# Kernel optimization log

Measured on AMD Instinct MI355X. Metric: run time of the kernel, lower is better.

## Reference

```python
import jax, jax.numpy as jnp
import numpy as np

L, D, DFF, B = 8192, 768, 3072, 2  # seq len, model dim, ffn hidden (4*D), batch

def _ln(x, g, b):
    m = x.mean(-1, keepdims=True)
    v = ((x - m) ** 2).mean(-1, keepdims=True)
    return (x - m) / jnp.sqrt(v + 1e-5) * g + b

def _ffn(x, w1, b1, w2, b2):
    return jax.nn.silu(x @ w1 + b1) @ w2 + b2

def setup_inputs() -> dict:
    key = jax.random.key(0)
    ks = jax.random.split(key, 8)
    s = lambda k, shape: jax.random.normal(k, shape, dtype=jnp.float32) * 0.02
    return dict(
        z=jax.random.normal(ks[0], (B, L, D), dtype=jnp.float32),
        pos=s(ks[1], (L, D)),                      # learned positional encoding table
        a=jax.random.normal(ks[2], (1,), dtype=jnp.float32),
        w1p=s(ks[3], (D, DFF)), b1p=jnp.zeros((DFF,), jnp.float32),
        w2p=s(ks[4], (DFF, D)), b2p=jnp.zeros((D,), jnp.float32),
        w1=s(ks[5], (D, DFF)),  b1=jnp.zeros((DFF,), jnp.float32),
        w2=s(ks[6], (DFF, D)),  b2=jnp.zeros((D,), jnp.float32),
        gamma=jnp.ones((D,), jnp.float32),
        beta=jnp.zeros((D,), jnp.float32),
    )

def reference(z, pos, a, w1p, b1p, w2p, b2p, w1, b1, w2, b2, gamma, beta):
    Ls = z.shape[1]
    n = 2 * Ls  # zero-padded FFT length for linear (causal) convolution
    fz = jnp.fft.rfft(_ln(z, gamma, beta), n=n, axis=1)          # (B, L+1, D) complex
    h = _ffn(pos, w1p, b1p, w2p, b2p)                            # (L, D) implicit filter
    window = jnp.exp(-jnp.arange(Ls, dtype=jnp.float32) * jnp.exp(a[0]))  # (L,)
    wfh = jnp.fft.rfft(window[:, None] * h, n=n, axis=0)         # (L+1, D) complex
    conv = jnp.fft.irfft(wfh[None] * fz, n=n, axis=1)[:, :Ls]    # (B, L, D)
    z = conv + z
    z = _ffn(_ln(z, gamma, beta), w1, b1, w2, b2) + z
    return z
```

## Files before the change

kernel.cpp:

```cpp
#include <hip/hip_runtime.h>
#include <hip/hip_bf16.h>
#include <stdint.h>

typedef __hip_bfloat16 bf16;
typedef __bf16 bf16x8 __attribute__((ext_vector_type(8)));
typedef float f32x4 __attribute__((ext_vector_type(4)));

#define LQ   8192
#define DQ   768
#define DFFQ 3072
#define NF   8192
#define NFULL 16384
#define TWO_PI 6.2831853071795864769f

__device__ __forceinline__ float b2f(bf16 v) { return __bfloat162float(v); }
__device__ __forceinline__ bf16 f2b(float v) { return __float2bfloat16(v); }
__device__ __forceinline__ float ldf(const bf16& v) { return __bfloat162float(v); }
__device__ __forceinline__ float ldf(const float& v) { return v; }
__device__ __forceinline__ float2 cmul(float2 a, float2 b) {
    return make_float2(a.x * b.x - a.y * b.y, a.x * b.y + a.y * b.x);
}
__device__ __forceinline__ int rev13(int k) { return (int)(__brev((unsigned)k) >> 19); }

__device__ __forceinline__ void glds16(const bf16* g, unsigned short* l) {
    __builtin_amdgcn_global_load_lds(
        (const __attribute__((address_space(1))) void*)g,
        (__attribute__((address_space(3))) void*)l, 16, 0, 0);
}

__global__ __launch_bounds__(256) void cast_f32_bf16(const float* __restrict__ in,
                                                     bf16* __restrict__ out, int n) {
    int i = (blockIdx.x * 256 + threadIdx.x) * 4;
    if (i + 3 < n) {
        float4 v = *(const float4*)(in + i);
        out[i] = f2b(v.x); out[i + 1] = f2b(v.y);
        out[i + 2] = f2b(v.z); out[i + 3] = f2b(v.w);
    }
}

template <typename TIN>
__global__ __launch_bounds__(256) void ln_kernel(const TIN* __restrict__ x,
                                                 const float* __restrict__ gamma,
                                                 const float* __restrict__ beta,
                                                 bf16* __restrict__ y) {
    size_t row = blockIdx.x;
    const TIN* xr = x + row * DQ;
    int tid = threadIdx.x;
    float v0 = ldf(xr[tid]), v1 = ldf(xr[tid + 256]), v2 = ldf(xr[tid + 512]);
    float s = v0 + v1 + v2;
    float sq = v0 * v0 + v1 * v1 + v2 * v2;
    for (int o = 32; o > 0; o >>= 1) {
        s += __shfl_down(s, o, 64);
        sq += __shfl_down(sq, o, 64);
    }
    __shared__ float red[8];
    __shared__ float mi[2];
    int lane = tid & 63, wid = tid >> 6;
    if (lane == 0) { red[wid] = s; red[4 + wid] = sq; }
    __syncthreads();
    if (tid == 0) {
        float ts = red[0] + red[1] + red[2] + red[3];
        float tq = red[4] + red[5] + red[6] + red[7];
        float mean = ts * (1.0f / 768.0f);
        float var = tq * (1.0f / 768.0f) - mean * mean;
        mi[0] = mean;
        mi[1] = rsqrtf(var + 1e-5f);
    }
    __syncthreads();
    float mean = mi[0], inv = mi[1];
    bf16* yr = y + row * DQ;
    yr[tid]       = f2b((v0 - mean) * inv * gamma[tid]       + beta[tid]);
    yr[tid + 256] = f2b((v1 - mean) * inv * gamma[tid + 256] + beta[tid + 256]);
    yr[tid + 512] = f2b((v2 - mean) * inv * gamma[tid + 512] + beta[tid + 512]);
}

template <typename TIN>
__global__ __launch_bounds__(256) void transpose_to_bf16(const TIN* __restrict__ in,
                                                         bf16* __restrict__ out,
                                                         int R, int C) {
    __shared__ bf16 tile[32][33];
    size_t base = (size_t)blockIdx.z * (size_t)R * (size_t)C;
    int c0 = blockIdx.x * 32, r0 = blockIdx.y * 32;
    int x = threadIdx.x, ty = threadIdx.y;
    for (int i = ty; i < 32; i += 8)
        tile[i][x] = f2b(ldf(in[base + (size_t)(r0 + i) * C + c0 + x]));
    __syncthreads();
    for (int i = ty; i < 32; i += 8)
        out[base + (size_t)(c0 + i) * R + r0 + x] = tile[x][i];
}

__global__ __launch_bounds__(256) void transpose_window(const float* __restrict__ h,
                                                        const float* __restrict__ a,
                                                        float* __restrict__ whT) {
    __shared__ float tile[32][33];
    float rate = expf(a[0]);
    int d0 = blockIdx.x * 32, t0 = blockIdx.y * 32;
    int x = threadIdx.x, ty = threadIdx.y;
    for (int i = ty; i < 32; i += 8) {
        int t = t0 + i;
        tile[i][x] = h[(size_t)t * DQ + d0 + x] * expf(-(float)t * rate);
    }
    __syncthreads();
    for (int i = ty; i < 32; i += 8)
        whT[(size_t)(d0 + i) * LQ + t0 + x] = tile[x][i];
}

__global__ __launch_bounds__(256) void transpose_residual(const bf16* __restrict__ convT,
                                                          const float* __restrict__ z,
                                                          bf16* __restrict__ z2) {
    __shared__ bf16 tile[32][33];
    size_t cbase = (size_t)blockIdx.z * DQ * LQ;
    size_t zbase = (size_t)blockIdx.z * LQ * DQ;
    int t0 = blockIdx.x * 32, d0 = blockIdx.y * 32;
    int x = threadIdx.x, ty = threadIdx.y;
    for (int i = ty; i < 32; i += 8)
        tile[i][x] = convT[cbase + (size_t)(d0 + i) * LQ + t0 + x];
    __syncthreads();
    for (int i = ty; i < 32; i += 8) {
        size_t idx = zbase + (size_t)(t0 + i) * DQ + d0 + x;
        z2[idx] = f2b(b2f(tile[x][i]) + z[idx]);
    }
}

__device__ __forceinline__ void fft_dif8192(float2* s) {
    const int tid = threadIdx.x;
    for (int half = 4096; half >= 1; half >>= 1) {
        float base = -TWO_PI / (float)(half * 2);
        for (int m = tid; m < 4096; m += 1024) {
            int j = m & (half - 1);
            int i0 = ((m - j) << 1) + j;
            int i1 = i0 + half;
            float2 u = s[i0], v = s[i1];
            float sn, cs;
            __sincosf(base * (float)j, &sn, &cs);
            s[i0] = make_float2(u.x + v.x, u.y + v.y);
            float dx = u.x - v.x, dy = u.y - v.y;
            s[i1] = make_float2(dx * cs - dy * sn, dx * sn + dy * cs);
        }
        __syncthreads();
    }
}
__device__ __forceinline__ void fft_dit8192(float2* s) {
    const int tid = threadIdx.x;
    for (int half = 1; half <= 4096; half <<= 1) {
        float base = TWO_PI / (float)(half * 2);
        for (int m = tid; m < 4096; m += 1024) {
            int j = m & (half - 1);
            int i0 = ((m - j) << 1) + j;
            int i1 = i0 + half;
            float2 u = s[i0], v = s[i1];
            float sn, cs;
            __sincosf(base * (float)j, &sn, &cs);
            float2 tv = make_float2(v.x * cs - v.y * sn, v.x * sn + v.y * cs);
            s[i0] = make_float2(u.x + tv.x, u.y + tv.y);
            s[i1] = make_float2(u.x - tv.x, u.y - tv.y);
        }
        __syncthreads();
    }
}

__global__ __launch_bounds__(1024) void filter_fft(const float* __restrict__ whT,
                                                   float2* __restrict__ H) {
    __shared__ float2 s[NF];
    int p = blockIdx.x;
    int d0 = 2 * p, d1 = d0 + 1;
    const float* x0 = whT + (size_t)d0 * LQ;
    const float* x1 = whT + (size_t)d1 * LQ;
    float2* H0 = H + (size_t)d0 * 8193;
    float2* H1 = H + (size_t)d1 * 8193;
    int tid = threadIdx.x;
    for (int t = tid; t < NF; t += 1024) s[t] = make_float2(x0[t], x1[t]);
    __syncthreads();
    fft_dif8192(s);
    for (int m = tid; m <= 4096; m += 1024) {
        int p1 = rev13(m), p2 = rev13((NF - m) & (NF - 1));
        float2 u = s[p1], v = s[p2];
        H0[2 * m] = make_float2(0.5f * (u.x + v.x), 0.5f * (u.y - v.y));
        H1[2 * m] = make_float2(0.5f * (u.y + v.y), 0.5f * (v.x - u.x));
    }
    __syncthreads();
    for (int t = tid; t < NF; t += 1024) {
        float sn, cs;
        __sincosf(-TWO_PI * (float)t / (float)NFULL, &sn, &cs);
        float2 xc = make_float2(x0[t], x1[t]);
        s[t] = make_float2(xc.x * cs - xc.y * sn, xc.x * sn + xc.y * cs);
    }
    __syncthreads();
    fft_dif8192(s);
    for (int m = tid; m < 4096; m += 1024) {
        int p1 = rev13(m), p2 = rev13(NF - 1 - m);
        float2 u = s[p1], v = s[p2];
        H0[2 * m + 1] = make_float2(0.5f * (u.x + v.x), 0.5f * (u.y - v.y));
        H1[2 * m + 1] = make_float2(0.5f * (u.y + v.y), 0.5f * (v.x - u.x));
    }
}

__global__ __launch_bounds__(1024) void fft_conv(const bf16* __restrict__ xlnT,
                                                 const float2* __restrict__ H,
                                                 bf16* __restrict__ convT) {
    __shared__ float2 s[NF];
    int wg = blockIdx.x;
    int b = wg / 384, p = wg % 384;
    int d0 = 2 * p, d1 = d0 + 1;
    const bf16* x0 = xlnT + ((size_t)b * DQ + d0) * LQ;
    const bf16* x1 = x0 + LQ;
    const float2* H0 = H + (size_t)d0 * 8193;
    const float2* H1 = H + (size_t)d1 * 8193;
    bf16* o0 = convT + ((size_t)b * DQ + d0) * LQ;
    bf16* o1 = o0 + LQ;
    int tid = threadIdx.x;

    for (int t = tid; t < NF; t += 1024) s[t] = make_float2(b2f(x0[t]), b2f(x1[t]));
    __syncthreads();
    fft_dif8192(s);
    for (int m = tid; m <= 4096; m += 1024) {
        int p1 = rev13(m), p2 = rev13((NF - m) & (NF - 1));
        float2 u = s[p1], v = s[p2];
        float2 X0 = make_float2(0.5f * (u.x + v.x), 0.5f * (u.y - v.y));
        float2 X1 = make_float2(0.5f * (u.y + v.y), 0.5f * (v.x - u.x));
        float2 Y0 = cmul(H0[2 * m], X0);
        float2 Y1 = cmul(H1[2 * m], X1);
        s[p1] = make_float2(Y0.x - Y1.y, Y0.y + Y1.x);
        s[p2] = make_float2(Y0.x + Y1.y, Y1.x - Y0.y);
    }
    __syncthreads();
    fft_dit8192(s);
    float2 e[8];
    for (int i = 0; i < 8; i++) e[i] = s[tid + 1024 * i];
    __syncthreads();

    for (int t = tid; t < NF; t += 1024) {
        float sn, cs;
        __sincosf(-TWO_PI * (float)t / (float)NFULL, &sn, &cs);
        float xv0 = b2f(x0[t]), xv1 = b2f(x1[t]);
        s[t] = make_float2(xv0 * cs - xv1 * sn, xv0 * sn + xv1 * cs);
    }
    __syncthreads();
    fft_dif8192(s);
    for (int m = tid; m < 4096; m += 1024) {
        int p1 = rev13(m), p2 = rev13(NF - 1 - m);
        float2 u = s[p1], v = s[p2];
        float2 X0 = make_float2(0.5f * (u.x + v.x), 0.5f * (u.y - v.y));
        float2 X1 = make_float2(0.5f * (u.y + v.y), 0.5f * (v.x - u.x));
        float2 Y0 = cmul(H0[2 * m + 1], X0);
        float2 Y1 = cmul(H1[2 * m + 1], X1);
        s[p1] = make_float2(Y0.x - Y1.y, Y0.y + Y1.x);
        s[p2] = make_float2(Y0.x + Y1.y, Y1.x - Y0.y);
    }
    __syncthreads();
    fft_dit8192(s);
    const float sc = 1.0f / (float)NFULL;
    for (int i = 0; i < 8; i++) {
        int t = tid + 1024 * i;
        float sn, cs;
        __sincosf(TWO_PI * (float)t / (float)NFULL, &sn, &cs);
        float2 o = s[t];
        float2 ot = make_float2(o.x * cs - o.y * sn, o.x * sn + o.y * cs);
        o0[t] = f2b((e[i].x + ot.x) * sc);
        o1[t] = f2b((e[i].y + ot.y) * sc);
    }
}

#define BMT 128
#define BNT 128
#define BKT 32

template <int EPI>
__global__ __launch_bounds__(256) void gemm_bt(const bf16* __restrict__ A,
                                               const bf16* __restrict__ Bt,
                                               const float* __restrict__ bias,
                                               const bf16* __restrict__ res,
                                               void* __restrict__ out,
                                               int M, int N, int K) {
    __shared__ __align__(16) unsigned short As[BMT * BKT];
    __shared__ __align__(16) unsigned short Bs[BNT * BKT];
    int tid = threadIdx.x;
    int m0 = blockIdx.y * BMT, n0 = blockIdx.x * BNT;
    int lane = tid & 63, w = tid >> 6;
    int wm = w >> 1, wn = w & 1;
    int colq = lane & 15, quad = lane >> 4;

    f32x4 acc[4][4];
    for (int i = 0; i < 4; i++)
        for (int j = 0; j < 4; j++) acc[i][j] = (f32x4){0.f, 0.f, 0.f, 0.f};

    int lrow = lane >> 2, lcol = (lane & 3) * 8;
    int ch0 = w * 2, ch1 = w * 2 + 1;
    const bf16* ga0 = A + (size_t)(m0 + ch0 * 16 + lrow) * K + lcol;
    const bf16* ga1 = A + (size_t)(m0 + ch1 * 16 + lrow) * K + lcol;
    const bf16* gb0 = Bt + (size_t)(n0 + ch0 * 16 + lrow) * K + lcol;
    const bf16* gb1 = Bt + (size_t)(n0 + ch1 * 16 + lrow) * K + lcol;
    unsigned short* la0 = As + ch0 * 512;
    unsigned short* la1 = As + ch1 * 512;
    unsigned short* lb0 = Bs + ch0 * 512;
    unsigned short* lb1 = Bs + ch1 * 512;

    const int nk = K / BKT;
    for (int kb = 0; kb < nk; kb++) {
        int k0 = kb * BKT;
        __syncthreads();
        glds16(ga0 + k0, la0);
        glds16(ga1 + k0, la1);
        glds16(gb0 + k0, lb0);
        glds16(gb1 + k0, lb1);
        __syncthreads();
        bf16x8 af[4], bfr[4];
        for (int i = 0; i < 4; i++) {
            int mrow = wm * 64 + i * 16 + colq;
            af[i] = *(const bf16x8*)(&As[mrow * BKT + quad * 8]);
            int nrow = wn * 64 + i * 16 + colq;
            bfr[i] = *(const bf16x8*)(&Bs[nrow * BKT + quad * 8]);
        }
        for (int i = 0; i < 4; i++)
            for (int j = 0; j < 4; j++)
                acc[i][j] = __builtin_amdgcn_mfma_f32_16x16x32_bf16(af[i], bfr[j], acc[i][j], 0, 0, 0);
    }
    for (int j = 0; j < 4; j++) {
        int n = n0 + wn * 64 + j * 16 + colq;
        float bv = bias[n];
        for (int i = 0; i < 4; i++) {
            int mbase = m0 + wm * 64 + i * 16 + quad * 4;
            for (int r = 0; r < 4; r++) {
                int m = mbase + r;
                float v = acc[i][j][r] + bv;
                size_t idx = (size_t)m * N + n;
                if (EPI == 0) {
                    ((bf16*)out)[idx] = f2b(v / (1.0f + expf(-v)));
                } else if (EPI == 1) {
                    ((float*)out)[idx] = v;
                } else {
                    ((float*)out)[idx] = v + b2f(res[idx]);
                }
            }
        }
    }
}

extern "C" void kernel_launch(void* const* d_in, const int* in_sizes, int n_in,
                              void* d_out, int out_size, void* d_ws, size_t ws_size,
                              hipStream_t stream) {
    (void)in_sizes; (void)n_in; (void)out_size; (void)ws_size;
    const float* z     = (const float*)d_in[0];
    const float* pos   = (const float*)d_in[1];
    const float* a     = (const float*)d_in[2];
    const float* w1p   = (const float*)d_in[3];
    const float* b1p   = (const float*)d_in[4];
    const float* w2p   = (const float*)d_in[5];
    const float* b2p   = (const float*)d_in[6];
    const float* w1    = (const float*)d_in[7];
    const float* b1    = (const float*)d_in[8];
    const float* w2    = (const float*)d_in[9];
    const float* b2    = (const float*)d_in[10];
    const float* gamma = (const float*)d_in[11];
    const float* beta  = (const float*)d_in[12];
    float* out = (float*)d_out;
    char* ws = (char*)d_ws;

    bf16*   w1T   = (bf16*)  (ws + 0);
    bf16*   w2T   = (bf16*)  (ws + 4718592);
    bf16*   w1pT  = (bf16*)  (ws + 9437184);
    bf16*   w2pT  = (bf16*)  (ws + 14155776);
    bf16*   xlnT  = (bf16*)  (ws + 18874368);
    bf16*   act1  = (bf16*)  (ws + 44040192);
    float2* Hbuf  = (float2*)(ws + 44040192);
    bf16*   xln   = (bf16*)  (ws + 94377984);
    bf16*   posb  = (bf16*)  (ws + 119543808);
    float*  h     = (float*) (ws + 119543808);
    float*  whT   = (float*) (ws + 94377984);
    bf16*   convT = (bf16*)  (ws + 119543808);
    bf16*   z2    = (bf16*)  (ws + 94377984);
    bf16*   xb    = (bf16*)  (ws + 119543808);
    bf16*   act2  = (bf16*)  (ws + 18874368);

    dim3 tb(32, 8);
    transpose_to_bf16<float><<<dim3(DFFQ / 32, DQ / 32, 1), tb, 0, stream>>>(w1p, w1pT, DQ, DFFQ);
    transpose_to_bf16<float><<<dim3(DQ / 32, DFFQ / 32, 1), tb, 0, stream>>>(w2p, w2pT, DFFQ, DQ);
    transpose_to_bf16<float><<<dim3(DFFQ / 32, DQ / 32, 1), tb, 0, stream>>>(w1, w1T, DQ, DFFQ);
    transpose_to_bf16<float><<<dim3(DQ / 32, DFFQ / 32, 1), tb, 0, stream>>>(w2, w2T, DFFQ, DQ);
    cast_f32_bf16<<<(LQ * DQ / 4 + 255) / 256, 256, 0, stream>>>(pos, posb, LQ * DQ);
    ln_kernel<float><<<2 * LQ, 256, 0, stream>>>(z, gamma, beta, xln);
    transpose_to_bf16<bf16><<<dim3(DQ / 32, LQ / 32, 2), tb, 0, stream>>>(xln, xlnT, LQ, DQ);
    gemm_bt<0><<<dim3(DFFQ / BNT, LQ / BMT), 256, 0, stream>>>(posb, w1pT, b1p, nullptr, act1, LQ, DFFQ, DQ);
    gemm_bt<1><<<dim3(DQ / BNT, LQ / BMT), 256, 0, stream>>>(act1, w2pT, b2p, nullptr, h, LQ, DQ, DFFQ);
    transpose_window<<<dim3(DQ / 32, LQ / 32), tb, 0, stream>>>(h, a, whT);
    filter_fft<<<DQ / 2, 1024, 0, stream>>>(whT, Hbuf);
    fft_conv<<<2 * (DQ / 2), 1024, 0, stream>>>(xlnT, Hbuf, convT);
    transpose_residual<<<dim3(LQ / 32, DQ / 32, 2), tb, 0, stream>>>(convT, z, z2);
    ln_kernel<bf16><<<2 * LQ, 256, 0, stream>>>(z2, gamma, beta, xb);
    for (int b = 0; b < 2; b++) {
        const bf16* xbh = xb + (size_t)b * LQ * DQ;
        const bf16* z2h = z2 + (size_t)b * LQ * DQ;
        float* outh = out + (size_t)b * LQ * DQ;
        gemm_bt<0><<<dim3(DFFQ / BNT, LQ / BMT), 256, 0, stream>>>(xbh, w1T, b1, nullptr, act2, LQ, DFFQ, DQ);
        gemm_bt<2><<<dim3(DQ / BNT, LQ / BMT), 256, 0, stream>>>(act2, w2T, b2, z2h, outh, LQ, DQ, DFFQ);
    }
}
```

Measured before the change: 937.5 us.

## Replace radix-2 FFT stages with register radix-8 passes and swizzled LDS

Replaces the 13-stage radix-2 shared-memory FFT (one barrier and one LDS round trip per stage) with four radix-8 register passes plus a final shuffle-based radix-2 stage. Inputs and outputs stay in registers across the first and last passes. LDS indices are XOR-swizzled to avoid bank conflicts, and per-element sincos calls are replaced by a twiddle recurrence. The H spectrum is stored split into even and odd halves instead of interleaved. Barrier and LDS traffic drop sharply, in exchange for more register pressure and more complex indexing in a 1024-thread block.

```diff
diff --git a/kernel.cpp b/kernel.cpp
--- a/kernel.cpp
+++ b/kernel.cpp
@@ -12,6 +12,9 @@
 #define NF   8192
 #define NFULL 16384
 #define TWO_PI 6.2831853071795864769f
+#define RSQ2 0.70710678118654752f
+#define C16  0.92387953251128676f
+#define S16  0.38268343236508977f
 
 __device__ __forceinline__ float b2f(bf16 v) { return __bfloat162float(v); }
 __device__ __forceinline__ bf16 f2b(float v) { return __float2bfloat16(v); }
@@ -20,7 +23,11 @@
 __device__ __forceinline__ float2 cmul(float2 a, float2 b) {
     return make_float2(a.x * b.x - a.y * b.y, a.x * b.y + a.y * b.x);
 }
+__device__ __forceinline__ float2 csqr(float2 a) {
+    return make_float2(a.x * a.x - a.y * a.y, 2.f * a.x * a.y);
+}
 __device__ __forceinline__ int rev13(int k) { return (int)(__brev((unsigned)k) >> 19); }
+__device__ __forceinline__ int SWZ(int i) { return i ^ ((i >> 5) & 31) ^ ((i >> 9) & 15); }
 
 __device__ __forceinline__ void glds16(const bf16* g, unsigned short* l) {
     __builtin_amdgcn_global_load_lds(
@@ -122,40 +129,147 @@
     }
 }
 
-__device__ __forceinline__ void fft_dif8192(float2* s) {
+
+__device__ __forceinline__ void dif_bf(float2& u, float2& v, float2 tw) {
+    float2 a = make_float2(u.x + v.x, u.y + v.y);
+    float2 b = make_float2(u.x - v.x, u.y - v.y);
+    u = a; v = cmul(b, tw);
+}
+__device__ __forceinline__ void dit_bf(float2& u, float2& v, float2 tw) {
+    float2 tv = cmul(v, tw);
+    v = make_float2(u.x - tv.x, u.y - tv.y);
+    u = make_float2(u.x + tv.x, u.y + tv.y);
+}
+
+__device__ __forceinline__ void dif3(float2* x, float2 w) {
+    float2 w2 = csqr(w), w4 = csqr(w2);
+    float2 t1 = cmul(w, make_float2(RSQ2, -RSQ2));
+    float2 t2 = make_float2(w.y, -w.x);
+    float2 t3 = cmul(w, make_float2(-RSQ2, -RSQ2));
+    dif_bf(x[0], x[4], w);
+    dif_bf(x[1], x[5], t1);
+    dif_bf(x[2], x[6], t2);
+    dif_bf(x[3], x[7], t3);
+    float2 w2n = make_float2(w2.y, -w2.x);
+    dif_bf(x[0], x[2], w2);
+    dif_bf(x[1], x[3], w2n);
+    dif_bf(x[4], x[6], w2);
+    dif_bf(x[5], x[7], w2n);
+    dif_bf(x[0], x[1], w4);
+    dif_bf(x[2], x[3], w4);
+    dif_bf(x[4], x[5], w4);
+    dif_bf(x[6], x[7], w4);
+}
+__device__ __forceinline__ void dit3(float2* x, float2 w) {
+    float2 w2 = csqr(w), w4 = csqr(w2);
+    dit_bf(x[0], x[1], w4);
+    dit_bf(x[2], x[3], w4);
+    dit_bf(x[4], x[5], w4);
+    dit_bf(x[6], x[7], w4);
+    float2 w2p = make_float2(-w2.y, w2.x);
+    dit_bf(x[0], x[2], w2);
+    dit_bf(x[1], x[3], w2p);
+    dit_bf(x[4], x[6], w2);
+    dit_bf(x[5], x[7], w2p);
+    float2 t1 = cmul(w, make_float2(RSQ2, RSQ2));
+    float2 t2 = make_float2(-w.y, w.x);
+    float2 t3 = cmul(w, make_float2(-RSQ2, RSQ2));
+    dit_bf(x[0], x[4], w);
+    dit_bf(x[1], x[5], t1);
+    dit_bf(x[2], x[6], t2);
+    dit_bf(x[3], x[7], t3);
+}
+
+__device__ __forceinline__ void shfl_stage(float2* x, int l) {
+#pragma unroll
+    for (int i = 0; i < 8; i++) {
+        float ox = __shfl_xor(x[i].x, 1, 64);
+        float oy = __shfl_xor(x[i].y, 1, 64);
+        if (l == 0) { x[i].x += ox; x[i].y += oy; }
+        else        { x[i].x = ox - x[i].x; x[i].y = oy - x[i].y; }
+    }
+}
+
+__device__ __forceinline__ void fwd_fft(float2* s, float2* x) {
     const int tid = threadIdx.x;
-    for (int half = 4096; half >= 1; half >>= 1) {
-        float base = -TWO_PI / (float)(half * 2);
-        for (int m = tid; m < 4096; m += 1024) {
-            int j = m & (half - 1);
-            int i0 = ((m - j) << 1) + j;
-            int i1 = i0 + half;
-            float2 u = s[i0], v = s[i1];
-            float sn, cs;
-            __sincosf(base * (float)j, &sn, &cs);
-            s[i0] = make_float2(u.x + v.x, u.y + v.y);
-            float dx = u.x - v.x, dy = u.y - v.y;
-            s[i1] = make_float2(dx * cs - dy * sn, dx * sn + dy * cs);
-        }
-        __syncthreads();
-    }
-}
-__device__ __forceinline__ void fft_dit8192(float2* s) {
+    float sn, cs;
+    __sincosf(-(TWO_PI / 8192.f) * (float)tid, &sn, &cs);
+    dif3(x, make_float2(cs, sn));
+#pragma unroll
+    for (int i = 0; i < 8; i++) s[SWZ(tid + 1024 * i)] = x[i];
+    __syncthreads();
+    {
+        int l = tid & 127, base = (tid >> 7) * 1024 + l;
+#pragma unroll
+        for (int i = 0; i < 8; i++) x[i] = s[SWZ(base + 128 * i)];
+        __sincosf(-(TWO_PI / 1024.f) * (float)l, &sn, &cs);
+        dif3(x, make_float2(cs, sn));
+#pragma unroll
+        for (int i = 0; i < 8; i++) s[SWZ(base + 128 * i)] = x[i];
+    }
+    __syncthreads();
+    {
+        int l = tid & 15, base = (tid >> 4) * 128 + l;
+#pragma unroll
+        for (int i = 0; i < 8; i++) x[i] = s[SWZ(base + 16 * i)];
+        __sincosf(-(TWO_PI / 128.f) * (float)l, &sn, &cs);
+        dif3(x, make_float2(cs, sn));
+#pragma unroll
+        for (int i = 0; i < 8; i++) s[SWZ(base + 16 * i)] = x[i];
+    }
+    __syncthreads();
+    {
+        int l = tid & 1, base = (tid >> 1) * 16 + l;
+#pragma unroll
+        for (int i = 0; i < 8; i++) x[i] = s[SWZ(base + 2 * i)];
+        float2 w = l ? make_float2(C16, -S16) : make_float2(1.f, 0.f);
+        dif3(x, w);
+        shfl_stage(x, l);
+#pragma unroll
+        for (int i = 0; i < 8; i++) s[SWZ(base + 2 * i)] = x[i];
+    }
+    __syncthreads();
+}
+
+__device__ __forceinline__ void inv_fft(float2* s, float2* x) {
     const int tid = threadIdx.x;
-    for (int half = 1; half <= 4096; half <<= 1) {
-        float base = TWO_PI / (float)(half * 2);
-        for (int m = tid; m < 4096; m += 1024) {
-            int j = m & (half - 1);
-            int i0 = ((m - j) << 1) + j;
-            int i1 = i0 + half;
-            float2 u = s[i0], v = s[i1];
-            float sn, cs;
-            __sincosf(base * (float)j, &sn, &cs);
-            float2 tv = make_float2(v.x * cs - v.y * sn, v.x * sn + v.y * cs);
-            s[i0] = make_float2(u.x + tv.x, u.y + tv.y);
-            s[i1] = make_float2(u.x - tv.x, u.y - tv.y);
-        }
-        __syncthreads();
+    float sn, cs;
+    {
+        int l = tid & 1, base = (tid >> 1) * 16 + l;
+#pragma unroll
+        for (int i = 0; i < 8; i++) x[i] = s[SWZ(base + 2 * i)];
+        shfl_stage(x, l);
+        float2 w = l ? make_float2(C16, S16) : make_float2(1.f, 0.f);
+        dit3(x, w);
+#pragma unroll
+        for (int i = 0; i < 8; i++) s[SWZ(base + 2 * i)] = x[i];
+    }
+    __syncthreads();
+    {
+        int l = tid & 15, base = (tid >> 4) * 128 + l;
+#pragma unroll
+        for (int i = 0; i < 8; i++) x[i] = s[SWZ(base + 16 * i)];
+        __sincosf((TWO_PI / 128.f) * (float)l, &sn, &cs);
+        dit3(x, make_float2(cs, sn));
+#pragma unroll
+        for (int i = 0; i < 8; i++) s[SWZ(base + 16 * i)] = x[i];
+    }
+    __syncthreads();
+    {
+        int l = tid & 127, base = (tid >> 7) * 1024 + l;
+#pragma unroll
+        for (int i = 0; i < 8; i++) x[i] = s[SWZ(base + 128 * i)];
+        __sincosf((TWO_PI / 1024.f) * (float)l, &sn, &cs);
+        dit3(x, make_float2(cs, sn));
+#pragma unroll
+        for (int i = 0; i < 8; i++) s[SWZ(base + 128 * i)] = x[i];
+    }
+    __syncthreads();
+    {
+#pragma unroll
+        for (int i = 0; i < 8; i++) x[i] = s[SWZ(tid + 1024 * i)];
+        __sincosf((TWO_PI / 8192.f) * (float)tid, &sn, &cs);
+        dit3(x, make_float2(cs, sn));
     }
 }
 
@@ -169,29 +283,38 @@
     float2* H0 = H + (size_t)d0 * 8193;
     float2* H1 = H + (size_t)d1 * 8193;
     int tid = threadIdx.x;
-    for (int t = tid; t < NF; t += 1024) s[t] = make_float2(x0[t], x1[t]);
-    __syncthreads();
-    fft_dif8192(s);
+    float2 x[8];
+#pragma unroll
+    for (int i = 0; i < 8; i++) {
+        int t = tid + 1024 * i;
+        x[i] = make_float2(x0[t], x1[t]);
+    }
+    fwd_fft(s, x);
     for (int m = tid; m <= 4096; m += 1024) {
-        int p1 = rev13(m), p2 = rev13((NF - m) & (NF - 1));
+        int p1 = SWZ(rev13(m)), p2 = SWZ(rev13((NF - m) & (NF - 1)));
         float2 u = s[p1], v = s[p2];
-        H0[2 * m] = make_float2(0.5f * (u.x + v.x), 0.5f * (u.y - v.y));
-        H1[2 * m] = make_float2(0.5f * (u.y + v.y), 0.5f * (v.x - u.x));
-    }
-    __syncthreads();
-    for (int t = tid; t < NF; t += 1024) {
+        H0[m] = make_float2(0.5f * (u.x + v.x), 0.5f * (u.y - v.y));
+        H1[m] = make_float2(0.5f * (u.y + v.y), 0.5f * (v.x - u.x));
+    }
+    __syncthreads();
+    {
         float sn, cs;
-        __sincosf(-TWO_PI * (float)t / (float)NFULL, &sn, &cs);
-        float2 xc = make_float2(x0[t], x1[t]);
-        s[t] = make_float2(xc.x * cs - xc.y * sn, xc.x * sn + xc.y * cs);
-    }
-    __syncthreads();
-    fft_dif8192(s);
+        __sincosf(-(TWO_PI / 16384.f) * (float)tid, &sn, &cs);
+        float2 ch = make_float2(cs, sn);
+        const float2 stepm = make_float2(C16, -S16);
+#pragma unroll
+        for (int i = 0; i < 8; i++) {
+            int t = tid + 1024 * i;
+            x[i] = cmul(make_float2(x0[t], x1[t]), ch);
+            ch = cmul(ch, stepm);
+        }
+    }
+    fwd_fft(s, x);
     for (int m = tid; m < 4096; m += 1024) {
-        int p1 = rev13(m), p2 = rev13(NF - 1 - m);
+        int p1 = SWZ(rev13(m)), p2 = SWZ(rev13(NF - 1 - m));
         float2 u = s[p1], v = s[p2];
-        H0[2 * m + 1] = make_float2(0.5f * (u.x + v.x), 0.5f * (u.y - v.y));
-        H1[2 * m + 1] = make_float2(0.5f * (u.y + v.y), 0.5f * (v.x - u.x));
+        H0[4097 + m] = make_float2(0.5f * (u.x + v.x), 0.5f * (u.y - v.y));
+        H1[4097 + m] = make_float2(0.5f * (u.y + v.y), 0.5f * (v.x - u.x));
     }
 }
 
@@ -209,55 +332,70 @@
     bf16* o0 = convT + ((size_t)b * DQ + d0) * LQ;
     bf16* o1 = o0 + LQ;
     int tid = threadIdx.x;
-
-    for (int t = tid; t < NF; t += 1024) s[t] = make_float2(b2f(x0[t]), b2f(x1[t]));
-    __syncthreads();
-    fft_dif8192(s);
+    float2 x[8];
+
+#pragma unroll
+    for (int i = 0; i < 8; i++) {
+        int t = tid + 1024 * i;
+        x[i] = make_float2(b2f(x0[t]), b2f(x1[t]));
+    }
+    fwd_fft(s, x);
     for (int m = tid; m <= 4096; m += 1024) {
-        int p1 = rev13(m), p2 = rev13((NF - m) & (NF - 1));
+        int p1 = SWZ(rev13(m)), p2 = SWZ(rev13((NF - m) & (NF - 1)));
         float2 u = s[p1], v = s[p2];
         float2 X0 = make_float2(0.5f * (u.x + v.x), 0.5f * (u.y - v.y));
         float2 X1 = make_float2(0.5f * (u.y + v.y), 0.5f * (v.x - u.x));
-        float2 Y0 = cmul(H0[2 * m], X0);
-        float2 Y1 = cmul(H1[2 * m], X1);
+        float2 Y0 = cmul(H0[m], X0);
+        float2 Y1 = cmul(H1[m], X1);
         s[p1] = make_float2(Y0.x - Y1.y, Y0.y + Y1.x);
         s[p2] = make_float2(Y0.x + Y1.y, Y1.x - Y0.y);
     }
     __syncthreads();
-    fft_dit8192(s);
+    inv_fft(s, x);
     float2 e[8];
-    for (int i = 0; i < 8; i++) e[i] = s[tid + 1024 * i];
-    __syncthreads();
-
-    for (int t = tid; t < NF; t += 1024) {
+#pragma unroll
+    for (int i = 0; i < 8; i++) e[i] = x[i];
+    __syncthreads();
+
+    {
         float sn, cs;
-        __sincosf(-TWO_PI * (float)t / (float)NFULL, &sn, &cs);
-        float xv0 = b2f(x0[t]), xv1 = b2f(x1[t]);
-        s[t] = make_float2(xv0 * cs - xv1 * sn, xv0 * sn + xv1 * cs);
-    }
-    __syncthreads();
-    fft_dif8192(s);
+        __sincosf(-(TWO_PI / 16384.f) * (float)tid, &sn, &cs);
+        float2 ch = make_float2(cs, sn);
+        const float2 stepm = make_float2(C16, -S16);
+#pragma unroll
+        for (int i = 0; i < 8; i++) {
+            int t = tid + 1024 * i;
+            x[i] = cmul(make_float2(b2f(x0[t]), b2f(x1[t])), ch);
+            ch = cmul(ch, stepm);
+        }
+    }
+    fwd_fft(s, x);
     for (int m = tid; m < 4096; m += 1024) {
-        int p1 = rev13(m), p2 = rev13(NF - 1 - m);
+        int p1 = SWZ(rev13(m)), p2 = SWZ(rev13(NF - 1 - m));
         float2 u = s[p1], v = s[p2];
         float2 X0 = make_float2(0.5f * (u.x + v.x), 0.5f * (u.y - v.y));
         float2 X1 = make_float2(0.5f * (u.y + v.y), 0.5f * (v.x - u.x));
-        float2 Y0 = cmul(H0[2 * m + 1], X0);
-        float2 Y1 = cmul(H1[2 * m + 1], X1);
+        float2 Y0 = cmul(H0[4097 + m], X0);
+        float2 Y1 = cmul(H1[4097 + m], X1);
         s[p1] = make_float2(Y0.x - Y1.y, Y0.y + Y1.x);
         s[p2] = make_float2(Y0.x + Y1.y, Y1.x - Y0.y);
     }
     __syncthreads();
-    fft_dit8192(s);
-    const float sc = 1.0f / (float)NFULL;
-    for (int i = 0; i < 8; i++) {
-        int t = tid + 1024 * i;
+    inv_fft(s, x);
+    {
         float sn, cs;
-        __sincosf(TWO_PI * (float)t / (float)NFULL, &sn, &cs);
-        float2 o = s[t];
-        float2 ot = make_float2(o.x * cs - o.y * sn, o.x * sn + o.y * cs);
-        o0[t] = f2b((e[i].x + ot.x) * sc);
-        o1[t] = f2b((e[i].y + ot.y) * sc);
+        __sincosf((TWO_PI / 16384.f) * (float)tid, &sn, &cs);
+        float2 wr = make_float2(cs, sn);
+        const float2 stepp = make_float2(C16, S16);
+        const float sc = 1.0f / (float)NFULL;
+#pragma unroll
+        for (int i = 0; i < 8; i++) {
+            int t = tid + 1024 * i;
+            float2 ot = cmul(x[i], wr);
+            o0[t] = f2b((e[i].x + ot.x) * sc);
+            o1[t] = f2b((e[i].y + ot.y) * sc);
+            wr = cmul(wr, stepp);
+        }
     }
 }
 
```

Result: slower. 1.028 ms (+9.6%).

## Replace split 8192-point FFTs with single radix-4 16384-point FFT in shared memory

Applied to the files above, without the earlier changes.

Replaces the two half-length 8192-point FFT passes (even and odd bins) with one 16384-point FFT held in 128 KB of LDS. The transform uses radix-4 (two fused radix-2) stages and exploits the zero padding in the first forward and last inverse stage. An XOR swizzle on LDS indices is meant to cut bank conflicts. This roughly halves the number of barrier-separated stages and twiddle computations per convolution, but doubles LDS use per block, which may limit occupancy to one block per CU.

```diff
diff --git a/kernel.cpp b/kernel.cpp
--- a/kernel.cpp
+++ b/kernel.cpp
@@ -9,7 +9,6 @@
 #define LQ   8192
 #define DQ   768
 #define DFFQ 3072
-#define NF   8192
 #define NFULL 16384
 #define TWO_PI 6.2831853071795864769f
 
@@ -20,7 +19,11 @@
 __device__ __forceinline__ float2 cmul(float2 a, float2 b) {
     return make_float2(a.x * b.x - a.y * b.y, a.x * b.y + a.y * b.x);
 }
-__device__ __forceinline__ int rev13(int k) { return (int)(__brev((unsigned)k) >> 19); }
+__device__ __forceinline__ float2 csqr(float2 a) {
+    return make_float2(a.x * a.x - a.y * a.y, 2.f * a.x * a.y);
+}
+__device__ __forceinline__ int rev14(int k) { return (int)(__brev((unsigned)k) >> 18); }
+__device__ __forceinline__ int SWZ(int i) { return i ^ ((i >> 5) & 31) ^ ((i >> 9) & 15); }
 
 __device__ __forceinline__ void glds16(const bf16* g, unsigned short* l) {
     __builtin_amdgcn_global_load_lds(
@@ -122,38 +125,80 @@
     }
 }
 
-__device__ __forceinline__ void fft_dif8192(float2* s) {
+
+__device__ __forceinline__ void dif_bf(float2& u, float2& v, float2 tw) {
+    float2 a = make_float2(u.x + v.x, u.y + v.y);
+    float2 b = make_float2(u.x - v.x, u.y - v.y);
+    u = a; v = cmul(b, tw);
+}
+__device__ __forceinline__ void dit_bf(float2& u, float2& v, float2 tw) {
+    float2 tv = cmul(v, tw);
+    v = make_float2(u.x - tv.x, u.y - tv.y);
+    u = make_float2(u.x + tv.x, u.y + tv.y);
+}
+__device__ __forceinline__ void dif2(float2& x0, float2& x1, float2& x2, float2& x3,
+                                     float2 w) {
+    float2 w2 = csqr(w);
+    float2 wn = make_float2(w.y, -w.x);
+    dif_bf(x0, x2, w);
+    dif_bf(x1, x3, wn);
+    dif_bf(x0, x1, w2);
+    dif_bf(x2, x3, w2);
+}
+__device__ __forceinline__ void dit2(float2& x0, float2& x1, float2& x2, float2& x3,
+                                     float2 w) {
+    float2 w2 = csqr(w);
+    float2 wp = make_float2(-w.y, w.x);
+    dit_bf(x0, x1, w2);
+    dit_bf(x2, x3, w2);
+    dit_bf(x0, x2, w);
+    dit_bf(x1, x3, wp);
+}
+
+__device__ __forceinline__ void fwd_mid(float2* s) {
     const int tid = threadIdx.x;
-    for (int half = 4096; half >= 1; half >>= 1) {
-        float base = -TWO_PI / (float)(half * 2);
-        for (int m = tid; m < 4096; m += 1024) {
-            int j = m & (half - 1);
-            int i0 = ((m - j) << 1) + j;
-            int i1 = i0 + half;
-            float2 u = s[i0], v = s[i1];
-            float sn, cs;
-            __sincosf(base * (float)j, &sn, &cs);
-            s[i0] = make_float2(u.x + v.x, u.y + v.y);
-            float dx = u.x - v.x, dy = u.y - v.y;
-            s[i1] = make_float2(dx * cs - dy * sn, dx * sn + dy * cs);
+#pragma unroll
+    for (int k = 10; k >= 0; k -= 2) {
+        const int S = 1 << k;
+        for (int g2 = 0; g2 < 4; g2++) {
+            int G = tid + (g2 << 10);
+            int l = G & (S - 1);
+            int base = ((G >> k) << (k + 2)) | l;
+            float2 x0 = s[SWZ(base)];
+            float2 x1 = s[SWZ(base + S)];
+            float2 x2 = s[SWZ(base + 2 * S)];
+            float2 x3 = s[SWZ(base + 3 * S)];
+            float ang = -(TWO_PI * 0.25f / (float)S) * (float)l;
+            float2 w = make_float2(__cosf(ang), __sinf(ang));
+            dif2(x0, x1, x2, x3, w);
+            s[SWZ(base)] = x0;
+            s[SWZ(base + S)] = x1;
+            s[SWZ(base + 2 * S)] = x2;
+            s[SWZ(base + 3 * S)] = x3;
         }
         __syncthreads();
     }
 }
-__device__ __forceinline__ void fft_dit8192(float2* s) {
+__device__ __forceinline__ void inv_mid(float2* s) {
     const int tid = threadIdx.x;
-    for (int half = 1; half <= 4096; half <<= 1) {
-        float base = TWO_PI / (float)(half * 2);
-        for (int m = tid; m < 4096; m += 1024) {
-            int j = m & (half - 1);
-            int i0 = ((m - j) << 1) + j;
-            int i1 = i0 + half;
-            float2 u = s[i0], v = s[i1];
-            float sn, cs;
-            __sincosf(base * (float)j, &sn, &cs);
-            float2 tv = make_float2(v.x * cs - v.y * sn, v.x * sn + v.y * cs);
-            s[i0] = make_float2(u.x + tv.x, u.y + tv.y);
-            s[i1] = make_float2(u.x - tv.x, u.y - tv.y);
+#pragma unroll
+    for (int k = 0; k <= 10; k += 2) {
+        const int S = 1 << k;
+        for (int g2 = 0; g2 < 4; g2++) {
+            int G = tid + (g2 << 10);
+            int l = G & (S - 1);
+            int base = ((G >> k) << (k + 2)) | l;
+            float2 x0 = s[SWZ(base)];
+            float2 x1 = s[SWZ(base + S)];
+            float2 x2 = s[SWZ(base + 2 * S)];
+            float2 x3 = s[SWZ(base + 3 * S)];
+            float ang = (TWO_PI * 0.25f / (float)S) * (float)l;
+            float2 w = make_float2(__cosf(ang), __sinf(ang));
+            dit2(x0, x1, x2, x3, w);
+            s[SWZ(base)] = x0;
+            s[SWZ(base + S)] = x1;
+            s[SWZ(base + 2 * S)] = x2;
+            s[SWZ(base + 3 * S)] = x3;
         }
         __syncthreads();
     }
@@ -161,103 +206,111 @@
 
 __global__ __launch_bounds__(1024) void filter_fft(const float* __restrict__ whT,
                                                    float2* __restrict__ H) {
-    __shared__ float2 s[NF];
+    __shared__ float2 s[NFULL];
     int p = blockIdx.x;
     int d0 = 2 * p, d1 = d0 + 1;
-    const float* x0 = whT + (size_t)d0 * LQ;
-    const float* x1 = whT + (size_t)d1 * LQ;
+    const float* g0 = whT + (size_t)d0 * LQ;
+    const float* g1 = whT + (size_t)d1 * LQ;
     float2* H0 = H + (size_t)d0 * 8193;
     float2* H1 = H + (size_t)d1 * 8193;
-    int tid = threadIdx.x;
-    for (int t = tid; t < NF; t += 1024) s[t] = make_float2(x0[t], x1[t]);
-    __syncthreads();
-    fft_dif8192(s);
-    for (int m = tid; m <= 4096; m += 1024) {
-        int p1 = rev13(m), p2 = rev13((NF - m) & (NF - 1));
+    const int tid = threadIdx.x;
+
+    for (int g2 = 0; g2 < 4; g2++) {
+        int G = tid + (g2 << 10);
+        float2 x0 = make_float2(g0[G], g1[G]);
+        float2 x1 = make_float2(g0[G + 4096], g1[G + 4096]);
+        float ang = -(TWO_PI / 16384.f) * (float)G;
+        float2 w = make_float2(__cosf(ang), __sinf(ang));
+        float2 w2 = csqr(w);
+        float2 wn = make_float2(w.y, -w.x);
+        float2 x2 = cmul(x0, w);
+        float2 x3 = cmul(x1, wn);
+        dif_bf(x0, x1, w2);
+        dif_bf(x2, x3, w2);
+        s[SWZ(G)] = x0;
+        s[SWZ(G + 4096)] = x1;
+        s[SWZ(G + 8192)] = x2;
+        s[SWZ(G + 12288)] = x3;
+    }
+    __syncthreads();
+    fwd_mid(s);
+    for (int m = tid; m <= 8192; m += 1024) {
+        int p1 = SWZ(rev14(m)), p2 = SWZ(rev14((NFULL - m) & (NFULL - 1)));
         float2 u = s[p1], v = s[p2];
-        H0[2 * m] = make_float2(0.5f * (u.x + v.x), 0.5f * (u.y - v.y));
-        H1[2 * m] = make_float2(0.5f * (u.y + v.y), 0.5f * (v.x - u.x));
-    }
-    __syncthreads();
-    for (int t = tid; t < NF; t += 1024) {
-        float sn, cs;
-        __sincosf(-TWO_PI * (float)t / (float)NFULL, &sn, &cs);
-        float2 xc = make_float2(x0[t], x1[t]);
-        s[t] = make_float2(xc.x * cs - xc.y * sn, xc.x * sn + xc.y * cs);
-    }
-    __syncthreads();
-    fft_dif8192(s);
-    for (int m = tid; m < 4096; m += 1024) {
-        int p1 = rev13(m), p2 = rev13(NF - 1 - m);
-        float2 u = s[p1], v = s[p2];
-        H0[2 * m + 1] = make_float2(0.5f * (u.x + v.x), 0.5f * (u.y - v.y));
-        H1[2 * m + 1] = make_float2(0.5f * (u.y + v.y), 0.5f * (v.x - u.x));
+        H0[m] = make_float2(0.5f * (u.x + v.x), 0.5f * (u.y - v.y));
+        H1[m] = make_float2(0.5f * (u.y + v.y), 0.5f * (v.x - u.x));
     }
 }
 
 __global__ __launch_bounds__(1024) void fft_conv(const bf16* __restrict__ xlnT,
                                                  const float2* __restrict__ H,
                                                  bf16* __restrict__ convT) {
-    __shared__ float2 s[NF];
+    __shared__ float2 s[NFULL];
     int wg = blockIdx.x;
     int b = wg / 384, p = wg % 384;
     int d0 = 2 * p, d1 = d0 + 1;
-    const bf16* x0 = xlnT + ((size_t)b * DQ + d0) * LQ;
-    const bf16* x1 = x0 + LQ;
+    const bf16* g0 = xlnT + ((size_t)b * DQ + d0) * LQ;
+    const bf16* g1 = g0 + LQ;
     const float2* H0 = H + (size_t)d0 * 8193;
     const float2* H1 = H + (size_t)d1 * 8193;
     bf16* o0 = convT + ((size_t)b * DQ + d0) * LQ;
     bf16* o1 = o0 + LQ;
-    int tid = threadIdx.x;
-
-    for (int t = tid; t < NF; t += 1024) s[t] = make_float2(b2f(x0[t]), b2f(x1[t]));
-    __syncthreads();
-    fft_dif8192(s);
-    for (int m = tid; m <= 4096; m += 1024) {
-        int p1 = rev13(m), p2 = rev13((NF - m) & (NF - 1));
+    const int tid = threadIdx.x;
+
+    for (int g2 = 0; g2 < 4; g2++) {
+        int G = tid + (g2 << 10);
+        float2 x0 = make_float2(b2f(g0[G]), b2f(g1[G]));
+        float2 x1 = make_float2(b2f(g0[G + 4096]), b2f(g1[G + 4096]));
+        float ang = -(TWO_PI / 16384.f) * (float)G;
+        float2 w = make_float2(__cosf(ang), __sinf(ang));
+        float2 w2 = csqr(w);
+        float2 wn = make_float2(w.y, -w.x);
+        float2 x2 = cmul(x0, w);
+        float2 x3 = cmul(x1, wn);
+        dif_bf(x0, x1, w2);
+        dif_bf(x2, x3, w2);
+        s[SWZ(G)] = x0;
+        s[SWZ(G + 4096)] = x1;
+        s[SWZ(G + 8192)] = x2;
+        s[SWZ(G + 12288)] = x3;
+    }
+    __syncthreads();
+    fwd_mid(s);
+
+    for (int m = tid; m <= 8192; m += 1024) {
+        int p1 = SWZ(rev14(m)), p2 = SWZ(rev14((NFULL - m) & (NFULL - 1)));
         float2 u = s[p1], v = s[p2];
         float2 X0 = make_float2(0.5f * (u.x + v.x), 0.5f * (u.y - v.y));
         float2 X1 = make_float2(0.5f * (u.y + v.y), 0.5f * (v.x - u.x));
-        float2 Y0 = cmul(H0[2 * m], X0);
-        float2 Y1 = cmul(H1[2 * m], X1);
+        float2 Y0 = cmul(H0[m], X0);
+        float2 Y1 = cmul(H1[m], X1);
         s[p1] = make_float2(Y0.x - Y1.y, Y0.y + Y1.x);
         s[p2] = make_float2(Y0.x + Y1.y, Y1.x - Y0.y);
     }
     __syncthreads();
-    fft_dit8192(s);
-    float2 e[8];
-    for (int i = 0; i < 8; i++) e[i] = s[tid + 1024 * i];
-    __syncthreads();
-
-    for (int t = tid; t < NF; t += 1024) {
-        float sn, cs;
-        __sincosf(-TWO_PI * (float)t / (float)NFULL, &sn, &cs);
-        float xv0 = b2f(x0[t]), xv1 = b2f(x1[t]);
-        s[t] = make_float2(xv0 * cs - xv1 * sn, xv0 * sn + xv1 * cs);
-    }
-    __syncthreads();
-    fft_dif8192(s);
-    for (int m = tid; m < 4096; m += 1024) {
-        int p1 = rev13(m), p2 = rev13(NF - 1 - m);
-        float2 u = s[p1], v = s[p2];
-        float2 X0 = make_float2(0.5f * (u.x + v.x), 0.5f * (u.y - v.y));
-        float2 X1 = make_float2(0.5f * (u.y + v.y), 0.5f * (v.x - u.x));
-        float2 Y0 = cmul(H0[2 * m + 1], X0);
-        float2 Y1 = cmul(H1[2 * m + 1], X1);
-        s[p1] = make_float2(Y0.x - Y1.y, Y0.y + Y1.x);
-        s[p2] = make_float2(Y0.x + Y1.y, Y1.x - Y0.y);
-    }
-    __syncthreads();
-    fft_dit8192(s);
-    const float sc = 1.0f / (float)NFULL;
-    for (int i = 0; i < 8; i++) {
-        int t = tid + 1024 * i;
-        float sn, cs;
-        __sincosf(TWO_PI * (float)t / (float)NFULL, &sn, &cs);
-        float2 o = s[t];
-        float2 ot = make_float2(o.x * cs - o.y * sn, o.x * sn + o.y * cs);
-        o0[t] = f2b((e[i].x + ot.x) * sc);
-        o1[t] = f2b((e[i].y + ot.y) * sc);
+
+    inv_mid(s);
+    {
+        const float sc = 1.0f / (float)NFULL;
+        for (int g2 = 0; g2 < 4; g2++) {
+            int G = tid + (g2 << 10);
+            float2 x0 = s[SWZ(G)];
+            float2 x1 = s[SWZ(G + 4096)];
+            float2 x2 = s[SWZ(G + 8192)];
+            float2 x3 = s[SWZ(G + 12288)];
+            float ang = (TWO_PI / 16384.f) * (float)G;
+            float2 w = make_float2(__cosf(ang), __sinf(ang));
+            float2 w2 = csqr(w);
+            dit_bf(x0, x1, w2);
+            dit_bf(x2, x3, w2);
+            float2 t0 = cmul(x2, w);
+            float2 wp = make_float2(-w.y, w.x);
+            float2 t1 = cmul(x3, wp);
+            o0[G]        = f2b((x0.x + t0.x) * sc);
+            o1[G]        = f2b((x0.y + t0.y) * sc);
+            o0[G + 4096] = f2b((x1.x + t1.x) * sc);
+            o1[G + 4096] = f2b((x1.y + t1.y) * sc);
+        }
     }
 }
 
```

After: 818.5 us. 1.15x faster.
